# Kernel optimization log

Hardware: AMD Instinct MI355X
Metric: run time of the kernel (lower is better)

## Reference

```python
import jax, jax.numpy as jnp
import numpy as np

NUM_ITERATIONS = 3
NUM_SLOTS = 8
SLOT_SIZE = 256
MLP_HIDDEN = 512
EPSILON = 1e-8
LN_EPS = 1e-5


def _ln(x, w, b):
    m = jnp.mean(x, axis=-1, keepdims=True)
    v = jnp.var(x, axis=-1, keepdims=True)
    return (x - m) * jax.lax.rsqrt(v + LN_EPS) * w + b


def _gru_cell(x, h, w_ih, w_hh, b_ih, b_hh):
    # torch.nn.GRUCell semantics; gates ordered [r, z, n]
    gi = x @ w_ih.T + b_ih
    gh = h @ w_hh.T + b_hh
    ir, iz, inn = jnp.split(gi, 3, axis=-1)
    hr, hz, hn = jnp.split(gh, 3, axis=-1)
    r = jax.nn.sigmoid(ir + hr)
    z = jax.nn.sigmoid(iz + hz)
    n = jnp.tanh(inn + r * hn)
    return (1.0 - z) * n + z * h


def setup_inputs() -> dict:
    key = jax.random.key(0)
    ks = jax.random.split(key, 12)
    D, H = SLOT_SIZE, MLP_HIDDEN
    s = 0.02
    return {
        "inputs": jax.random.normal(ks[0], (64, 4096, D), dtype=jnp.float32),
        "noise": jax.random.normal(ks[1], (64, NUM_SLOTS, D), dtype=jnp.float32),
        "ln_in_w": jnp.ones((D,), jnp.float32), "ln_in_b": jnp.zeros((D,), jnp.float32),
        "ln_slots_w": jnp.ones((D,), jnp.float32), "ln_slots_b": jnp.zeros((D,), jnp.float32),
        "ln_mlp_w": jnp.ones((D,), jnp.float32), "ln_mlp_b": jnp.zeros((D,), jnp.float32),
        "slots_mu": jax.random.normal(ks[2], (1, 1, D), jnp.float32) * s,
        "slots_log_sigma": jnp.zeros((1, 1, D), jnp.float32),
        "Wq": jax.random.normal(ks[3], (D, D), jnp.float32) * s,
        "Wk": jax.random.normal(ks[4], (D, D), jnp.float32) * s,
        "Wv": jax.random.normal(ks[5], (D, D), jnp.float32) * s,
        "gru_w_ih": jax.random.normal(ks[6], (3 * D, D), jnp.float32) * s,
        "gru_w_hh": jax.random.normal(ks[7], (3 * D, D), jnp.float32) * s,
        "gru_b_ih": jnp.zeros((3 * D,), jnp.float32),
        "gru_b_hh": jnp.zeros((3 * D,), jnp.float32),
        "mlp_w1": jax.random.normal(ks[8], (H, D), jnp.float32) * s,
        "mlp_b1": jnp.zeros((H,), jnp.float32),
        "mlp_w2": jax.random.normal(ks[9], (D, H), jnp.float32) * s,
        "mlp_b2": jnp.zeros((D,), jnp.float32),
    }


def reference(inputs, noise, ln_in_w, ln_in_b, ln_slots_w, ln_slots_b, ln_mlp_w, ln_mlp_b,
              slots_mu, slots_log_sigma, Wq, Wk, Wv,
              gru_w_ih, gru_w_hh, gru_b_ih, gru_b_hh,
              mlp_w1, mlp_b1, mlp_w2, mlp_b2):
    B, N, D = inputs.shape
    S = NUM_SLOTS
    x = _ln(inputs, ln_in_w, ln_in_b)            # [B,N,D]
    k = x @ Wk.T                                  # [B,N,D]
    v = x @ Wv.T                                  # [B,N,D]
    slots = slots_mu + jnp.exp(slots_log_sigma) * noise   # [B,S,D]
    scale = D ** (-0.5)
    for _ in range(NUM_ITERATIONS):
        slots_prev = slots
        s_n = _ln(slots, ln_slots_w, ln_slots_b)
        q = (s_n @ Wq.T) * scale                  # [B,S,D]
        attn_logits = jnp.einsum('bnd,bsd->bns', k, q)
        attn = jax.nn.softmax(attn_logits, axis=-1) + EPSILON
        attn = attn / jnp.sum(attn, axis=-2, keepdims=True)   # renorm over inputs
        updates = jnp.einsum('bns,bnd->bsd', attn, v)          # [B,S,D]
        slots = _gru_cell(updates.reshape(-1, D), slots_prev.reshape(-1, D),
                          gru_w_ih, gru_w_hh, gru_b_ih, gru_b_hh).reshape(B, S, D)
        h = jax.nn.relu(_ln(slots, ln_mlp_w, ln_mlp_b) @ mlp_w1.T + mlp_b1)
        slots = slots + (h @ mlp_w2.T + mlp_b2)
    return slots
```

## Files before the change

kernel.cpp:

```cpp
#include <hip/hip_runtime.h>

#define CB 64
#define CN 4096
#define CD 256
#define CS 8
#define CH 512

typedef __bf16 bf16_t;
typedef bf16_t bf16x8 __attribute__((ext_vector_type(8)));
typedef float f32x4 __attribute__((ext_vector_type(4)));

__device__ __forceinline__ unsigned short f2bf(float f){
  unsigned int u = __builtin_bit_cast(unsigned int, f);
  u += 0x7FFFu + ((u >> 16) & 1u);
  return (unsigned short)(u >> 16);
}

__device__ __forceinline__ f32x4 mfma16(bf16x8 a, bf16x8 b, f32x4 c){
  return __builtin_amdgcn_mfma_f32_16x16x32_bf16(a, b, c, 0, 0, 0);
}

__device__ __forceinline__ void gl_lds16(const void* g, void* l){
  __builtin_amdgcn_global_load_lds(
      (const __attribute__((address_space(1))) unsigned int*)g,
      (__attribute__((address_space(3))) unsigned int*)l, 16, 0, 0);
}

__global__ __launch_bounds__(256) void k_ln(const float* __restrict__ in,
    const float* __restrict__ gw, const float* __restrict__ gb,
    unsigned short* __restrict__ x){
  int blk = blockIdx.x;
  int b = blk >> 6, nt = blk & 63;
  int wv = threadIdx.x >> 6, l = threadIdx.x & 63;
  const float* base = in + ((size_t)b*CN + (size_t)nt*64) * CD;
  unsigned short* xb = x + ((size_t)b*CN + (size_t)nt*64) * CD;
  float4 w4 = *(const float4*)(gw + 4*l);
  float4 b4 = *(const float4*)(gb + 4*l);
  for(int i = 0; i < 16; i++){
    int r = wv*16 + i;
    float4 v = *(const float4*)(base + (size_t)r*CD + 4*l);
    float s1 = v.x + v.y + v.z + v.w;
    float s2 = v.x*v.x + v.y*v.y + v.z*v.z + v.w*v.w;
    #pragma unroll
    for(int m = 1; m < 64; m <<= 1){ s1 += __shfl_xor(s1, m); s2 += __shfl_xor(s2, m); }
    float mean = s1 * (1.0f/CD);
    float var  = fmaxf(s2 * (1.0f/CD) - mean*mean, 0.0f);
    float rstd = rsqrtf(var + 1e-5f);
    float y0 = (v.x - mean)*rstd*w4.x + b4.x;
    float y1 = (v.y - mean)*rstd*w4.y + b4.y;
    float y2 = (v.z - mean)*rstd*w4.z + b4.z;
    float y3 = (v.w - mean)*rstd*w4.w + b4.w;
    uint2 p;
    p.x = (unsigned)f2bf(y0) | ((unsigned)f2bf(y1) << 16);
    p.y = (unsigned)f2bf(y2) | ((unsigned)f2bf(y3) << 16);
    *(uint2*)(xb + (size_t)r*CD + 4*l) = p;
  }
}

__global__ __launch_bounds__(256) void k_setup(
    const float* __restrict__ Wq, const float* __restrict__ Wk,
    const float* __restrict__ wih, const float* __restrict__ Wv,
    const float* __restrict__ whh, const float* __restrict__ w1,
    const float* __restrict__ w2, const float* __restrict__ noise,
    const float* __restrict__ mu, const float* __restrict__ lsig,
    unsigned short* __restrict__ M1T, unsigned short* __restrict__ Mih_bf,
    unsigned short* __restrict__ Whh_bf, unsigned short* __restrict__ w1_bf,
    unsigned short* __restrict__ w2_bf, float* __restrict__ slots){
  int bid = blockIdx.x, tid = threadIdx.x;
  if(bid < 256){
    int ep = bid, e = tid;
    float acc = 0.0f;
    for(int d = 0; d < 256; d++) acc = fmaf(Wq[(size_t)d*256 + e], Wk[(size_t)d*256 + ep], acc);
    M1T[(size_t)ep*256 + e] = f2bf(acc * 0.0625f);
  } else if(bid < 1024){
    int j = bid - 256, e = tid;
    float acc = 0.0f;
    for(int d = 0; d < 256; d++) acc = fmaf(wih[(size_t)j*256 + d], Wv[(size_t)d*256 + e], acc);
    Mih_bf[(size_t)j*256 + e] = f2bf(acc);
  } else if(bid < 1792){
    int idx = (bid - 1024)*256 + tid;
    Whh_bf[idx] = f2bf(whh[idx]);
  } else if(bid < 2304){
    int idx = (bid - 1792)*256 + tid;
    w1_bf[idx] = f2bf(w1[idx]);
  } else if(bid < 2816){
    int idx = (bid - 2304)*256 + tid;
    w2_bf[idx] = f2bf(w2[idx]);
  } else {
    int idx = (bid - 2816)*256 + tid;
    int d = idx & 255;
    slots[idx] = mu[d] + __expf(lsig[d]) * noise[idx];
  }
}

__global__ __launch_bounds__(256) void k_qt(const float* __restrict__ slots,
    const float* __restrict__ lw, const float* __restrict__ lb,
    const unsigned short* __restrict__ M1T, unsigned short* __restrict__ qt,
    float* __restrict__ U, float* __restrict__ den){
  __shared__ unsigned short sn[16*264];
  int b = blockIdx.x;
  int tid = threadIdx.x;
  float4 z4 = {0.f, 0.f, 0.f, 0.f};
  float* Ub = U + (size_t)b*CS*CD;
  *(float4*)(Ub + tid*8)     = z4;
  *(float4*)(Ub + tid*8 + 4) = z4;
  if(tid < CS) den[b*CS + tid] = 0.0f;

  int wv = tid >> 6, l = tid & 63;
  int lm = l & 15, lg = l >> 4;
  float4 w4 = *(const float4*)(lw + 4*l);
  float4 b4 = *(const float4*)(lb + 4*l);
  for(int i = 0; i < 2; i++){
    int r = wv*2 + i;
    float4 v = *(const float4*)(slots + ((size_t)b*CS + r)*CD + 4*l);
    float s1 = v.x + v.y + v.z + v.w;
    float s2 = v.x*v.x + v.y*v.y + v.z*v.z + v.w*v.w;
    #pragma unroll
    for(int m = 1; m < 64; m <<= 1){ s1 += __shfl_xor(s1, m); s2 += __shfl_xor(s2, m); }
    float mean = s1 * (1.0f/CD);
    float var  = fmaxf(s2 * (1.0f/CD) - mean*mean, 0.0f);
    float rstd = rsqrtf(var + 1e-5f);
    float y0 = (v.x - mean)*rstd*w4.x + b4.x;
    float y1 = (v.y - mean)*rstd*w4.y + b4.y;
    float y2 = (v.z - mean)*rstd*w4.z + b4.z;
    float y3 = (v.w - mean)*rstd*w4.w + b4.w;
    uint2 p;
    p.x = (unsigned)f2bf(y0) | ((unsigned)f2bf(y1) << 16);
    p.y = (unsigned)f2bf(y2) | ((unsigned)f2bf(y3) << 16);
    *(uint2*)(&sn[r*264 + 4*l]) = p;
    uint2 zz; zz.x = 0u; zz.y = 0u;
    *(uint2*)(&sn[(r+8)*264 + 4*l]) = zz;
  }
  __syncthreads();
  bf16x8 af[8];
  #pragma unroll
  for(int k = 0; k < 8; k++) af[k] = *(const bf16x8*)(&sn[lm*264 + k*32 + lg*8]);
  #pragma unroll
  for(int ntile = 0; ntile < 4; ntile++){
    int ep = wv*64 + ntile*16 + lm;
    f32x4 acc = {0.f, 0.f, 0.f, 0.f};
    const unsigned short* mrow = M1T + (size_t)ep*CD;
    #pragma unroll
    for(int k = 0; k < 8; k++){
      bf16x8 bf = *(const bf16x8*)(mrow + k*32 + lg*8);
      acc = mfma16(af[k], bf, acc);
    }
    #pragma unroll
    for(int reg = 0; reg < 4; reg++){
      int s = lg*4 + reg;
      qt[((size_t)b*16 + s)*CD + ep] = f2bf(acc[reg]);
    }
  }
}

__global__ __launch_bounds__(256) void k_attn(const unsigned short* __restrict__ x,
    const unsigned short* __restrict__ qt, float* __restrict__ U, float* __restrict__ den){
  __shared__ unsigned short xt[64*256];
  __shared__ unsigned short pt[16*72];
  int b = blockIdx.x >> 4, chunk = blockIdx.x & 15;
  int wv = threadIdx.x >> 6, l = threadIdx.x & 63;
  int lm = l & 15, lg = l >> 4;

  bf16x8 qb[8];
  const unsigned short* qrow = qt + ((size_t)b*16 + lm)*CD;
  #pragma unroll
  for(int k = 0; k < 8; k++) qb[k] = *(const bf16x8*)(qrow + k*32 + lg*8);

  f32x4 uacc[4];
  #pragma unroll
  for(int nt = 0; nt < 4; nt++){ f32x4 z = {0.f,0.f,0.f,0.f}; uacc[nt] = z; }
  float dacc = 0.0f;

  const unsigned short* xbatch = x + (size_t)b*CN*CD + (size_t)chunk*256*CD;

  for(int t = 0; t < 4; t++){
    const unsigned short* xtile = xbatch + (size_t)t*64*CD;
    __syncthreads();
    #pragma unroll
    for(int k2 = 0; k2 < 8; k2++){
      int r0 = wv*16 + k2*2;
      int row = r0 + (l >> 5);
      int c = l & 31;
      int f = (row ^ (row >> 3)) & 7;
      const unsigned short* g = xtile + (size_t)row*CD + (size_t)(c ^ f)*8;
      gl_lds16(g, &xt[r0*CD]);
    }
    __syncthreads();

    f32x4 c4 = {0.f, 0.f, 0.f, 0.f};
    int rowl = wv*16 + lm;
    int f1 = (rowl ^ (rowl >> 3)) & 7;
    #pragma unroll
    for(int k = 0; k < 8; k++){
      int cc = (k*4 + lg) ^ f1;
      bf16x8 a = *(const bf16x8*)(&xt[rowl*256 + cc*8]);
      c4 = mfma16(a, qb[k], c4);
    }
    float pv[4];
    #pragma unroll
    for(int reg = 0; reg < 4; reg++){
      float v = (lm < 8) ? c4[reg] : -1e30f;
      float mx = v;
      #pragma unroll
      for(int m = 1; m < 16; m <<= 1) mx = fmaxf(mx, __shfl_xor(mx, m));
      float e = __expf(v - mx);
      float s = e;
      #pragma unroll
      for(int m = 1; m < 16; m <<= 1) s += __shfl_xor(s, m);
      float p = (lm < 8) ? (e/s + 1e-8f) : 0.0f;
      dacc += p;
      pv[reg] = p;
    }
    int rbase = wv*16 + lg*4;
    unsigned int p01 = (unsigned)f2bf(pv[0]) | ((unsigned)f2bf(pv[1]) << 16);
    unsigned int p23 = (unsigned)f2bf(pv[2]) | ((unsigned)f2bf(pv[3]) << 16);
    *(unsigned int*)(&pt[lm*72 + rbase])     = p01;
    *(unsigned int*)(&pt[lm*72 + rbase + 2]) = p23;
    __syncthreads();

    #pragma unroll
    for(int ks = 0; ks < 2; ks++){
      bf16x8 a = *(const bf16x8*)(&pt[lm*72 + ks*32 + lg*8]);
      int rb = ks*32 + lg*8;
      #pragma unroll
      for(int nt = 0; nt < 4; nt++){
        int e = wv*64 + nt*16 + lm;
        bf16x8 bfr;
        #pragma unroll
        for(int j = 0; j < 8; j++){
          int row2 = rb + j;
          int f2 = (row2 ^ (row2 >> 3)) & 7;
          int cidx = (e >> 3) ^ f2;
          unsigned short tv = xt[row2*256 + cidx*8 + (e & 7)];
          bfr[j] = __builtin_bit_cast(bf16_t, tv);
        }
        uacc[nt] = mfma16(a, bfr, uacc[nt]);
      }
    }
  }

  dacc += __shfl_xor(dacc, 16);
  dacc += __shfl_xor(dacc, 32);
  if(l < 8) atomicAdd(&den[b*CS + l], dacc);
  if(lg < 2){
    #pragma unroll
    for(int nt = 0; nt < 4; nt++){
      #pragma unroll
      for(int reg = 0; reg < 4; reg++){
        int s = lg*4 + reg;
        atomicAdd(&U[((size_t)b*CS + s)*CD + wv*64 + nt*16 + lm], uacc[nt][reg]);
      }
    }
  }
}

template<int EPI>
__global__ __launch_bounds__(256) void k_gemm_bf(
    const float* __restrict__ A, const unsigned short* __restrict__ Bt,
    float* __restrict__ C, int K, int N, int ntn,
    const float* __restrict__ bias, const float* __restrict__ res,
    const float* __restrict__ A2, const unsigned short* __restrict__ Bt2,
    float* __restrict__ C2){
  __shared__ unsigned short As[64*72];
  __shared__ unsigned short Bs[64*72];
  if(blockIdx.y == 1){ A = A2; Bt = Bt2; C = C2; }
  int bm = blockIdx.x / ntn, bn = blockIdx.x % ntn;
  int m0 = bm*64, n0 = bn*64;
  int tid = threadIdx.x;
  int wv = tid >> 6, l = tid & 63, lm = l & 15, lg = l >> 4;
  int sr = tid >> 2, sc = (tid & 3)*8;

  f32x4 acc[4];
  #pragma unroll
  for(int nt = 0; nt < 4; nt++){ f32x4 z = {0.f,0.f,0.f,0.f}; acc[nt] = z; }

  for(int k0 = 0; k0 < K; k0 += 32){
    __syncthreads();
    {
      const float* src = A + (size_t)(m0 + sr)*K + k0 + sc;
      float4 a0 = *(const float4*)(src);
      float4 a1 = *(const float4*)(src + 4);
      uint4 pk;
      pk.x = (unsigned)f2bf(a0.x) | ((unsigned)f2bf(a0.y) << 16);
      pk.y = (unsigned)f2bf(a0.z) | ((unsigned)f2bf(a0.w) << 16);
      pk.z = (unsigned)f2bf(a1.x) | ((unsigned)f2bf(a1.y) << 16);
      pk.w = (unsigned)f2bf(a1.z) | ((unsigned)f2bf(a1.w) << 16);
      *(uint4*)(&As[sr*72 + sc]) = pk;
      uint4 bv = *(const uint4*)(Bt + (size_t)(n0 + sr)*K + k0 + sc);
      *(uint4*)(&Bs[sr*72 + sc]) = bv;
    }
    __syncthreads();
    bf16x8 af = *(const bf16x8*)(&As[(wv*16 + lm)*72 + lg*8]);
    #pragma unroll
    for(int nt = 0; nt < 4; nt++){
      bf16x8 bf = *(const bf16x8*)(&Bs[(nt*16 + lm)*72 + lg*8]);
      acc[nt] = mfma16(af, bf, acc[nt]);
    }
  }

  #pragma unroll
  for(int nt = 0; nt < 4; nt++){
    int n = n0 + nt*16 + lm;
    float bi = (EPI != 0) ? bias[n] : 0.0f;
    #pragma unroll
    for(int reg = 0; reg < 4; reg++){
      int m = m0 + wv*16 + lg*4 + reg;
      float vv = acc[nt][reg];
      if(EPI == 1) vv = fmaxf(vv + bi, 0.0f);
      else if(EPI == 2) vv = vv + bi + res[(size_t)m*N + n];
      C[(size_t)m*N + n] = vv;
    }
  }
}

__global__ __launch_bounds__(256) void k_act(const float* __restrict__ gi,
    const float* __restrict__ gh, const float* __restrict__ den,
    const float* __restrict__ slots, const float* __restrict__ bih,
    const float* __restrict__ bhh, const float* __restrict__ lw,
    const float* __restrict__ lb, float* __restrict__ hp, float* __restrict__ lnh){
  int wv = threadIdx.x >> 6, l = threadIdx.x & 63;
  int row = blockIdx.x*4 + wv;
  const float* gir = gi + (size_t)row*768;
  const float* ghr = gh + (size_t)row*768;
  float invd = 1.0f / den[row];
  float4 air = *(const float4*)(gir + 4*l);
  float4 aiz = *(const float4*)(gir + 256 + 4*l);
  float4 ain = *(const float4*)(gir + 512 + 4*l);
  float4 ahr = *(const float4*)(ghr + 4*l);
  float4 ahz = *(const float4*)(ghr + 256 + 4*l);
  float4 ahn = *(const float4*)(ghr + 512 + 4*l);
  float4 br = *(const float4*)(bih + 4*l);
  float4 bz = *(const float4*)(bih + 256 + 4*l);
  float4 bn = *(const float4*)(bih + 512 + 4*l);
  float4 cr = *(const float4*)(bhh + 4*l);
  float4 cz = *(const float4*)(bhh + 256 + 4*l);
  float4 cn = *(const float4*)(bhh + 512 + 4*l);
  float4 hc = *(const float4*)(slots + (size_t)row*256 + 4*l);
  float4 h;
  #pragma unroll
  for(int i = 0; i < 4; i++){
    float gr = (&air.x)[i]*invd + (&br.x)[i] + (&ahr.x)[i] + (&cr.x)[i];
    float gz = (&aiz.x)[i]*invd + (&bz.x)[i] + (&ahz.x)[i] + (&cz.x)[i];
    float gn = (&ain.x)[i]*invd + (&bn.x)[i];
    float hn = (&ahn.x)[i] + (&cn.x)[i];
    float r = 1.0f/(1.0f + __expf(-gr));
    float z = 1.0f/(1.0f + __expf(-gz));
    float n = tanhf(gn + r*hn);
    (&h.x)[i] = (1.0f - z)*n + z*(&hc.x)[i];
  }
  *(float4*)(hp + (size_t)row*256 + 4*l) = h;
  float s1 = h.x + h.y + h.z + h.w;
  float s2 = h.x*h.x + h.y*h.y + h.z*h.z + h.w*h.w;
  #pragma unroll
  for(int m = 1; m < 64; m <<= 1){ s1 += __shfl_xor(s1, m); s2 += __shfl_xor(s2, m); }
  float mean = s1 * (1.0f/CD);
  float var  = fmaxf(s2 * (1.0f/CD) - mean*mean, 0.0f);
  float rstd = rsqrtf(var + 1e-5f);
  float4 w4 = *(const float4*)(lw + 4*l);
  float4 b4 = *(const float4*)(lb + 4*l);
  float4 o;
  o.x = (h.x - mean)*rstd*w4.x + b4.x;
  o.y = (h.y - mean)*rstd*w4.y + b4.y;
  o.z = (h.z - mean)*rstd*w4.z + b4.z;
  o.w = (h.w - mean)*rstd*w4.w + b4.w;
  *(float4*)(lnh + (size_t)row*256 + 4*l) = o;
}

extern "C" void kernel_launch(void* const* d_in, const int* in_sizes, int n_in,
                              void* d_out, int out_size, void* d_ws, size_t ws_size,
                              hipStream_t stream){
  const float* inputs = (const float*)d_in[0];
  const float* noise  = (const float*)d_in[1];
  const float* ln_in_w = (const float*)d_in[2];
  const float* ln_in_b = (const float*)d_in[3];
  const float* ln_sl_w = (const float*)d_in[4];
  const float* ln_sl_b = (const float*)d_in[5];
  const float* ln_ml_w = (const float*)d_in[6];
  const float* ln_ml_b = (const float*)d_in[7];
  const float* mu   = (const float*)d_in[8];
  const float* lsig = (const float*)d_in[9];
  const float* Wq  = (const float*)d_in[10];
  const float* Wk  = (const float*)d_in[11];
  const float* Wv  = (const float*)d_in[12];
  const float* wih = (const float*)d_in[13];
  const float* whh = (const float*)d_in[14];
  const float* bih = (const float*)d_in[15];
  const float* bhh = (const float*)d_in[16];
  const float* w1  = (const float*)d_in[17];
  const float* b1  = (const float*)d_in[18];
  const float* w2  = (const float*)d_in[19];
  const float* b2  = (const float*)d_in[20];

  char* ws = (char*)d_ws;
  size_t off = 0;
  unsigned short* x = (unsigned short*)(ws + off); off += (size_t)CB*CN*CD*2;
  float* slots = (float*)(ws + off); off += (size_t)CB*CS*CD*4;
  float* hp    = (float*)(ws + off); off += (size_t)CB*CS*CD*4;
  float* U     = (float*)(ws + off); off += (size_t)CB*CS*CD*4;
  float* den   = (float*)(ws + off); off += (size_t)CB*CS*4;
  unsigned short* qt     = (unsigned short*)(ws + off); off += (size_t)CB*16*CD*2;
  unsigned short* M1T    = (unsigned short*)(ws + off); off += (size_t)CD*CD*2;
  unsigned short* Mih_bf = (unsigned short*)(ws + off); off += (size_t)768*CD*2;
  unsigned short* Whh_bf = (unsigned short*)(ws + off); off += (size_t)768*CD*2;
  unsigned short* w1_bf  = (unsigned short*)(ws + off); off += (size_t)CH*CD*2;
  unsigned short* w2_bf  = (unsigned short*)(ws + off); off += (size_t)CD*CH*2;
  float* gi   = (float*)(ws + off); off += (size_t)512*768*4;
  float* gh   = (float*)(ws + off); off += (size_t)512*768*4;
  float* lnh  = (float*)(ws + off); off += (size_t)512*256*4;
  float* h1   = (float*)(ws + off); off += (size_t)512*512*4;

  k_ln<<<4096, 256, 0, stream>>>(inputs, ln_in_w, ln_in_b, x);
  k_setup<<<3328, 256, 0, stream>>>(Wq, Wk, wih, Wv, whh, w1, w2, noise, mu, lsig,
                                    M1T, Mih_bf, Whh_bf, w1_bf, w2_bf, slots);

  for(int it = 0; it < 3; it++){
    k_qt<<<64, 256, 0, stream>>>(slots, ln_sl_w, ln_sl_b, M1T, qt, U, den);
    k_attn<<<1024, 256, 0, stream>>>(x, qt, U, den);
    k_gemm_bf<0><<<dim3(96, 2), 256, 0, stream>>>(
        U, Mih_bf, gi, 256, 768, 12, nullptr, nullptr,
        slots, Whh_bf, gh);
    k_act<<<128, 256, 0, stream>>>(gi, gh, den, slots, bih, bhh, ln_ml_w, ln_ml_b, hp, lnh);
    k_gemm_bf<1><<<dim3(64, 1), 256, 0, stream>>>(
        lnh, w1_bf, h1, 256, 512, 8, b1, nullptr,
        nullptr, nullptr, nullptr);
    float* cdst = (it == 2) ? (float*)d_out : slots;
    k_gemm_bf<2><<<dim3(32, 1), 256, 0, stream>>>(
        h1, w2_bf, cdst, 512, 256, 4, b2, hp,
        nullptr, nullptr, nullptr);
  }
}
```

Before: 668.1 us.

## Fuse GRU, MLP and next-iteration query projection into one per-batch kernel

Replaces the per-iteration chain of GRU gemm, activation/layernorm, two MLP gemms and query-projection launches with a single k_update kernel: one block per batch element keeps all intermediates in LDS and runs the MFMA tiles directly from global bf16 weights. It also computes the next iteration's slot layernorm and query projection and clears the U/den accumulators, so k_qt now runs only once, before the loop. This removes several kernel launches and the global round-trips through the gi/gh/lnh/h1 buffers. In exchange only 64 blocks run, and each block streams the full weight matrices from cache with no sharing, so the fused kernel may be latency-bound.

```diff
diff --git a/kernel.cpp b/kernel.cpp
--- a/kernel.cpp
+++ b/kernel.cpp
@@ -254,116 +254,214 @@
   }
 }
 
-template<int EPI>
-__global__ __launch_bounds__(256) void k_gemm_bf(
-    const float* __restrict__ A, const unsigned short* __restrict__ Bt,
-    float* __restrict__ C, int K, int N, int ntn,
-    const float* __restrict__ bias, const float* __restrict__ res,
-    const float* __restrict__ A2, const unsigned short* __restrict__ Bt2,
-    float* __restrict__ C2){
-  __shared__ unsigned short As[64*72];
-  __shared__ unsigned short Bs[64*72];
-  if(blockIdx.y == 1){ A = A2; Bt = Bt2; C = C2; }
-  int bm = blockIdx.x / ntn, bn = blockIdx.x % ntn;
-  int m0 = bm*64, n0 = bn*64;
-  int tid = threadIdx.x;
-  int wv = tid >> 6, l = tid & 63, lm = l & 15, lg = l >> 4;
-  int sr = tid >> 2, sc = (tid & 3)*8;
-
-  f32x4 acc[4];
-  #pragma unroll
-  for(int nt = 0; nt < 4; nt++){ f32x4 z = {0.f,0.f,0.f,0.f}; acc[nt] = z; }
-
-  for(int k0 = 0; k0 < K; k0 += 32){
-    __syncthreads();
-    {
-      const float* src = A + (size_t)(m0 + sr)*K + k0 + sc;
-      float4 a0 = *(const float4*)(src);
-      float4 a1 = *(const float4*)(src + 4);
-      uint4 pk;
-      pk.x = (unsigned)f2bf(a0.x) | ((unsigned)f2bf(a0.y) << 16);
-      pk.y = (unsigned)f2bf(a0.z) | ((unsigned)f2bf(a0.w) << 16);
-      pk.z = (unsigned)f2bf(a1.x) | ((unsigned)f2bf(a1.y) << 16);
-      pk.w = (unsigned)f2bf(a1.z) | ((unsigned)f2bf(a1.w) << 16);
-      *(uint4*)(&As[sr*72 + sc]) = pk;
-      uint4 bv = *(const uint4*)(Bt + (size_t)(n0 + sr)*K + k0 + sc);
-      *(uint4*)(&Bs[sr*72 + sc]) = bv;
-    }
-    __syncthreads();
-    bf16x8 af = *(const bf16x8*)(&As[(wv*16 + lm)*72 + lg*8]);
-    #pragma unroll
-    for(int nt = 0; nt < 4; nt++){
-      bf16x8 bf = *(const bf16x8*)(&Bs[(nt*16 + lm)*72 + lg*8]);
-      acc[nt] = mfma16(af, bf, acc[nt]);
-    }
-  }
-
-  #pragma unroll
-  for(int nt = 0; nt < 4; nt++){
-    int n = n0 + nt*16 + lm;
-    float bi = (EPI != 0) ? bias[n] : 0.0f;
-    #pragma unroll
-    for(int reg = 0; reg < 4; reg++){
-      int m = m0 + wv*16 + lg*4 + reg;
-      float vv = acc[nt][reg];
-      if(EPI == 1) vv = fmaxf(vv + bi, 0.0f);
-      else if(EPI == 2) vv = vv + bi + res[(size_t)m*N + n];
-      C[(size_t)m*N + n] = vv;
-    }
-  }
-}
-
-__global__ __launch_bounds__(256) void k_act(const float* __restrict__ gi,
-    const float* __restrict__ gh, const float* __restrict__ den,
-    const float* __restrict__ slots, const float* __restrict__ bih,
-    const float* __restrict__ bhh, const float* __restrict__ lw,
-    const float* __restrict__ lb, float* __restrict__ hp, float* __restrict__ lnh){
-  int wv = threadIdx.x >> 6, l = threadIdx.x & 63;
-  int row = blockIdx.x*4 + wv;
-  const float* gir = gi + (size_t)row*768;
-  const float* ghr = gh + (size_t)row*768;
-  float invd = 1.0f / den[row];
-  float4 air = *(const float4*)(gir + 4*l);
-  float4 aiz = *(const float4*)(gir + 256 + 4*l);
-  float4 ain = *(const float4*)(gir + 512 + 4*l);
-  float4 ahr = *(const float4*)(ghr + 4*l);
-  float4 ahz = *(const float4*)(ghr + 256 + 4*l);
-  float4 ahn = *(const float4*)(ghr + 512 + 4*l);
-  float4 br = *(const float4*)(bih + 4*l);
-  float4 bz = *(const float4*)(bih + 256 + 4*l);
-  float4 bn = *(const float4*)(bih + 512 + 4*l);
-  float4 cr = *(const float4*)(bhh + 4*l);
-  float4 cz = *(const float4*)(bhh + 256 + 4*l);
-  float4 cn = *(const float4*)(bhh + 512 + 4*l);
-  float4 hc = *(const float4*)(slots + (size_t)row*256 + 4*l);
-  float4 h;
-  #pragma unroll
-  for(int i = 0; i < 4; i++){
-    float gr = (&air.x)[i]*invd + (&br.x)[i] + (&ahr.x)[i] + (&cr.x)[i];
-    float gz = (&aiz.x)[i]*invd + (&bz.x)[i] + (&ahz.x)[i] + (&cz.x)[i];
-    float gn = (&ain.x)[i]*invd + (&bn.x)[i];
-    float hn = (&ahn.x)[i] + (&cn.x)[i];
-    float r = 1.0f/(1.0f + __expf(-gr));
-    float z = 1.0f/(1.0f + __expf(-gz));
-    float n = tanhf(gn + r*hn);
-    (&h.x)[i] = (1.0f - z)*n + z*(&hc.x)[i];
-  }
-  *(float4*)(hp + (size_t)row*256 + 4*l) = h;
-  float s1 = h.x + h.y + h.z + h.w;
-  float s2 = h.x*h.x + h.y*h.y + h.z*h.z + h.w*h.w;
-  #pragma unroll
-  for(int m = 1; m < 64; m <<= 1){ s1 += __shfl_xor(s1, m); s2 += __shfl_xor(s2, m); }
-  float mean = s1 * (1.0f/CD);
-  float var  = fmaxf(s2 * (1.0f/CD) - mean*mean, 0.0f);
-  float rstd = rsqrtf(var + 1e-5f);
-  float4 w4 = *(const float4*)(lw + 4*l);
-  float4 b4 = *(const float4*)(lb + 4*l);
-  float4 o;
-  o.x = (h.x - mean)*rstd*w4.x + b4.x;
-  o.y = (h.y - mean)*rstd*w4.y + b4.y;
-  o.z = (h.z - mean)*rstd*w4.z + b4.z;
-  o.w = (h.w - mean)*rstd*w4.w + b4.w;
-  *(float4*)(lnh + (size_t)row*256 + 4*l) = o;
+__global__ __launch_bounds__(256) void k_update(
+    const float* __restrict__ U, const float* slots,
+    const float* __restrict__ den,
+    const unsigned short* __restrict__ Mih, const unsigned short* __restrict__ Whh,
+    const unsigned short* __restrict__ w1b, const unsigned short* __restrict__ w2b,
+    const unsigned short* __restrict__ M1T,
+    const float* __restrict__ bih, const float* __restrict__ bhh,
+    const float* __restrict__ lmw, const float* __restrict__ lmb,
+    const float* __restrict__ b1, const float* __restrict__ b2,
+    const float* __restrict__ lsw, const float* __restrict__ lsb,
+    float* out, unsigned short* __restrict__ qt,
+    float* __restrict__ Uz, float* __restrict__ denz, int last){
+  __shared__ unsigned short A1[16*264];
+  __shared__ unsigned short SBf[16*264];
+  __shared__ unsigned short A3[16*520];
+  __shared__ float G1[8*777];
+  __shared__ float G2[8*777];
+  __shared__ float Hh[8*257];
+  __shared__ float SN[8*257];
+  int b = blockIdx.x, tid = threadIdx.x;
+  int l = tid & 63, lm = l & 15, lg = l >> 4;
+  int wv = tid >> 6;
+
+  for(int i = tid; i < 8*264; i += 256){ A1[8*264 + i] = 0; SBf[8*264 + i] = 0; }
+  for(int i = tid; i < 8*520; i += 256) A3[8*520 + i] = 0;
+  {
+    int r = tid >> 5, c = (tid & 31)*8;
+    const float* Ur = U + ((size_t)b*CS + r)*CD + c;
+    float4 a0 = *(const float4*)Ur, a1 = *(const float4*)(Ur + 4);
+    uint4 pk;
+    pk.x = (unsigned)f2bf(a0.x) | ((unsigned)f2bf(a0.y) << 16);
+    pk.y = (unsigned)f2bf(a0.z) | ((unsigned)f2bf(a0.w) << 16);
+    pk.z = (unsigned)f2bf(a1.x) | ((unsigned)f2bf(a1.y) << 16);
+    pk.w = (unsigned)f2bf(a1.z) | ((unsigned)f2bf(a1.w) << 16);
+    *(uint4*)(&A1[r*264 + c]) = pk;
+    const float* Sr = slots + ((size_t)b*CS + r)*CD + c;
+    a0 = *(const float4*)Sr; a1 = *(const float4*)(Sr + 4);
+    pk.x = (unsigned)f2bf(a0.x) | ((unsigned)f2bf(a0.y) << 16);
+    pk.y = (unsigned)f2bf(a0.z) | ((unsigned)f2bf(a0.w) << 16);
+    pk.z = (unsigned)f2bf(a1.x) | ((unsigned)f2bf(a1.y) << 16);
+    pk.w = (unsigned)f2bf(a1.z) | ((unsigned)f2bf(a1.w) << 16);
+    *(uint4*)(&SBf[r*264 + c]) = pk;
+  }
+  __syncthreads();
+
+  {
+    bf16x8 afU[8], afS[8];
+    #pragma unroll
+    for(int k = 0; k < 8; k++){
+      afU[k] = *(const bf16x8*)(&A1[lm*264 + k*32 + lg*8]);
+      afS[k] = *(const bf16x8*)(&SBf[lm*264 + k*32 + lg*8]);
+    }
+    for(int t = 0; t < 12; t++){
+      int nb = wv*192 + t*16;
+      const unsigned short* br1 = Mih + (size_t)(nb + lm)*CD;
+      const unsigned short* br2 = Whh + (size_t)(nb + lm)*CD;
+      f32x4 ac1 = {0.f,0.f,0.f,0.f}, ac2 = {0.f,0.f,0.f,0.f};
+      #pragma unroll
+      for(int k = 0; k < 8; k++){
+        bf16x8 bv1 = *(const bf16x8*)(br1 + k*32 + lg*8);
+        ac1 = mfma16(afU[k], bv1, ac1);
+        bf16x8 bv2 = *(const bf16x8*)(br2 + k*32 + lg*8);
+        ac2 = mfma16(afS[k], bv2, ac2);
+      }
+      if(lg < 2){
+        #pragma unroll
+        for(int reg = 0; reg < 4; reg++){
+          int row = lg*4 + reg;
+          G1[row*777 + nb + lm] = ac1[reg];
+          G2[row*777 + nb + lm] = ac2[reg];
+        }
+      }
+    }
+  }
+  __syncthreads();
+
+  {
+    int r = tid >> 5, cl = tid & 31;
+    float invd = 1.0f / den[b*CS + r];
+    const float* srow = slots + ((size_t)b*CS + r)*CD;
+    float hv[8]; float s1 = 0.f, s2 = 0.f;
+    #pragma unroll
+    for(int i = 0; i < 8; i++){
+      int c = cl + 32*i;
+      float gr = G1[r*777 + c]*invd + bih[c] + G2[r*777 + c] + bhh[c];
+      float gz = G1[r*777 + 256 + c]*invd + bih[256 + c] + G2[r*777 + 256 + c] + bhh[256 + c];
+      float gn = G1[r*777 + 512 + c]*invd + bih[512 + c];
+      float hn = G2[r*777 + 512 + c] + bhh[512 + c];
+      float rr = 1.0f/(1.0f + __expf(-gr));
+      float zz = 1.0f/(1.0f + __expf(-gz));
+      float nn = tanhf(gn + rr*hn);
+      float h = (1.0f - zz)*nn + zz*srow[c];
+      hv[i] = h; Hh[r*257 + c] = h; s1 += h; s2 += h*h;
+    }
+    #pragma unroll
+    for(int m = 1; m < 32; m <<= 1){ s1 += __shfl_xor(s1, m); s2 += __shfl_xor(s2, m); }
+    float mean = s1 * (1.0f/CD);
+    float var  = fmaxf(s2 * (1.0f/CD) - mean*mean, 0.0f);
+    float rstd = rsqrtf(var + 1e-5f);
+    #pragma unroll
+    for(int i = 0; i < 8; i++){
+      int c = cl + 32*i;
+      A1[r*264 + c] = f2bf((hv[i] - mean)*rstd*lmw[c] + lmb[c]);
+    }
+  }
+  __syncthreads();
+
+  {
+    bf16x8 af[8];
+    #pragma unroll
+    for(int k = 0; k < 8; k++) af[k] = *(const bf16x8*)(&A1[lm*264 + k*32 + lg*8]);
+    for(int t = 0; t < 8; t++){
+      int nb = wv*128 + t*16;
+      const unsigned short* br = w1b + (size_t)(nb + lm)*CD;
+      f32x4 acc = {0.f,0.f,0.f,0.f};
+      #pragma unroll
+      for(int k = 0; k < 8; k++){
+        bf16x8 bv = *(const bf16x8*)(br + k*32 + lg*8);
+        acc = mfma16(af[k], bv, acc);
+      }
+      if(lg < 2){
+        int c = nb + lm;
+        float bb = b1[c];
+        #pragma unroll
+        for(int reg = 0; reg < 4; reg++)
+          A3[(lg*4 + reg)*520 + c] = f2bf(fmaxf(acc[reg] + bb, 0.0f));
+      }
+    }
+  }
+  __syncthreads();
+
+  {
+    bf16x8 af[16];
+    #pragma unroll
+    for(int k = 0; k < 16; k++) af[k] = *(const bf16x8*)(&A3[lm*520 + k*32 + lg*8]);
+    for(int t = 0; t < 4; t++){
+      int nb = wv*64 + t*16;
+      const unsigned short* br = w2b + (size_t)(nb + lm)*CH;
+      f32x4 acc = {0.f,0.f,0.f,0.f};
+      #pragma unroll
+      for(int k = 0; k < 16; k++){
+        bf16x8 bv = *(const bf16x8*)(br + k*32 + lg*8);
+        acc = mfma16(af[k], bv, acc);
+      }
+      if(lg < 2){
+        int c = nb + lm;
+        float bb = b2[c];
+        #pragma unroll
+        for(int reg = 0; reg < 4; reg++){
+          int row = lg*4 + reg;
+          float v = acc[reg] + bb + Hh[row*257 + c];
+          out[((size_t)b*CS + row)*CD + c] = v;
+          SN[row*257 + c] = v;
+        }
+      }
+    }
+  }
+  if(last) return;
+  __syncthreads();
+
+  {
+    int r = tid >> 5, cl = tid & 31;
+    float sv[8]; float s1 = 0.f, s2 = 0.f;
+    #pragma unroll
+    for(int i = 0; i < 8; i++){
+      int c = cl + 32*i;
+      float v = SN[r*257 + c]; sv[i] = v; s1 += v; s2 += v*v;
+    }
+    #pragma unroll
+    for(int m = 1; m < 32; m <<= 1){ s1 += __shfl_xor(s1, m); s2 += __shfl_xor(s2, m); }
+    float mean = s1 * (1.0f/CD);
+    float var  = fmaxf(s2 * (1.0f/CD) - mean*mean, 0.0f);
+    float rstd = rsqrtf(var + 1e-5f);
+    #pragma unroll
+    for(int i = 0; i < 8; i++){
+      int c = cl + 32*i;
+      A1[r*264 + c] = f2bf((sv[i] - mean)*rstd*lsw[c] + lsb[c]);
+    }
+  }
+  __syncthreads();
+  {
+    bf16x8 af[8];
+    #pragma unroll
+    for(int k = 0; k < 8; k++) af[k] = *(const bf16x8*)(&A1[lm*264 + k*32 + lg*8]);
+    for(int t = 0; t < 4; t++){
+      int nb = wv*64 + t*16;
+      const unsigned short* br = M1T + (size_t)(nb + lm)*CD;
+      f32x4 acc = {0.f,0.f,0.f,0.f};
+      #pragma unroll
+      for(int k = 0; k < 8; k++){
+        bf16x8 bv = *(const bf16x8*)(br + k*32 + lg*8);
+        acc = mfma16(af[k], bv, acc);
+      }
+      if(lg < 2){
+        int c = nb + lm;
+        #pragma unroll
+        for(int reg = 0; reg < 4; reg++)
+          qt[((size_t)b*16 + lg*4 + reg)*CD + c] = f2bf(acc[reg]);
+      }
+    }
+  }
+  {
+    float4 z4 = {0.f,0.f,0.f,0.f};
+    float* Ub = Uz + (size_t)b*CS*CD;
+    *(float4*)(Ub + tid*8)     = z4;
+    *(float4*)(Ub + tid*8 + 4) = z4;
+    if(tid < CS) denz[b*CS + tid] = 0.0f;
+  }
 }
 
 extern "C" void kernel_launch(void* const* d_in, const int* in_sizes, int n_in,
@@ -395,7 +493,6 @@
   size_t off = 0;
   unsigned short* x = (unsigned short*)(ws + off); off += (size_t)CB*CN*CD*2;
   float* slots = (float*)(ws + off); off += (size_t)CB*CS*CD*4;
-  float* hp    = (float*)(ws + off); off += (size_t)CB*CS*CD*4;
   float* U     = (float*)(ws + off); off += (size_t)CB*CS*CD*4;
   float* den   = (float*)(ws + off); off += (size_t)CB*CS*4;
   unsigned short* qt     = (unsigned short*)(ws + off); off += (size_t)CB*16*CD*2;
@@ -404,28 +501,18 @@
   unsigned short* Whh_bf = (unsigned short*)(ws + off); off += (size_t)768*CD*2;
   unsigned short* w1_bf  = (unsigned short*)(ws + off); off += (size_t)CH*CD*2;
   unsigned short* w2_bf  = (unsigned short*)(ws + off); off += (size_t)CD*CH*2;
-  float* gi   = (float*)(ws + off); off += (size_t)512*768*4;
-  float* gh   = (float*)(ws + off); off += (size_t)512*768*4;
-  float* lnh  = (float*)(ws + off); off += (size_t)512*256*4;
-  float* h1   = (float*)(ws + off); off += (size_t)512*512*4;
 
   k_ln<<<4096, 256, 0, stream>>>(inputs, ln_in_w, ln_in_b, x);
   k_setup<<<3328, 256, 0, stream>>>(Wq, Wk, wih, Wv, whh, w1, w2, noise, mu, lsig,
                                     M1T, Mih_bf, Whh_bf, w1_bf, w2_bf, slots);
+  k_qt<<<64, 256, 0, stream>>>(slots, ln_sl_w, ln_sl_b, M1T, qt, U, den);
 
   for(int it = 0; it < 3; it++){
-    k_qt<<<64, 256, 0, stream>>>(slots, ln_sl_w, ln_sl_b, M1T, qt, U, den);
     k_attn<<<1024, 256, 0, stream>>>(x, qt, U, den);
-    k_gemm_bf<0><<<dim3(96, 2), 256, 0, stream>>>(
-        U, Mih_bf, gi, 256, 768, 12, nullptr, nullptr,
-        slots, Whh_bf, gh);
-    k_act<<<128, 256, 0, stream>>>(gi, gh, den, slots, bih, bhh, ln_ml_w, ln_ml_b, hp, lnh);
-    k_gemm_bf<1><<<dim3(64, 1), 256, 0, stream>>>(
-        lnh, w1_bf, h1, 256, 512, 8, b1, nullptr,
-        nullptr, nullptr, nullptr);
-    float* cdst = (it == 2) ? (float*)d_out : slots;
-    k_gemm_bf<2><<<dim3(32, 1), 256, 0, stream>>>(
-        h1, w2_bf, cdst, 512, 256, 4, b2, hp,
-        nullptr, nullptr, nullptr);
-  }
-}
+    float* dst = (it == 2) ? (float*)d_out : slots;
+    k_update<<<64, 256, 0, stream>>>(U, slots, den,
+        Mih_bf, Whh_bf, w1_bf, w2_bf, M1T,
+        bih, bhh, ln_ml_w, ln_ml_b, b1, b2, ln_sl_w, ln_sl_b,
+        dst, qt, U, den, (it == 2) ? 1 : 0);
+  }
+}
```

New measurement: 711.0 us. +6.4%, slower.
